# Kernel tuning notes

Hardware: AMD Instinct MI355X
Metric: run time of the kernel (lower is better)

The kernel has to match this reference:

```python
import jax, jax.numpy as jnp
import numpy as np

GRID_SIZE = 8
MARGIN = 1.0
NUM_NEG = 4
SOS_NEG = 8
LOSS_LAMBDA = 1.0
IMG_H, IMG_W = 960, 1280  # desc2 is the stride-GRID_SIZE feature map of this image
BIG = 5.0    # fill for radius-masked entries in FOS distance matrix (> max unit-desc dist 2)
HUGE = 1e6   # fill for invalid entries in SOS candidate scores


def _l2n(x, eps=1e-8):
    return x / (jnp.linalg.norm(x, axis=-1, keepdims=True) + eps)


def _pdist(a, b, eps=1e-12):
    # a: B x N x C, b: B x M x C -> B x N x M euclidean distances
    sq = (jnp.sum(a * a, -1)[..., :, None] + jnp.sum(b * b, -1)[..., None, :]
          - 2.0 * jnp.einsum('bnc,bmc->bnm', a, b))
    return jnp.sqrt(jnp.maximum(sq, eps))


def _bilinear(desc, pts):
    # desc: B x C x H x W, pts: B x N x 2 in (y, x) image-pixel coords -> B x N x C
    B, C, H, W = desc.shape
    g = pts / GRID_SIZE - 0.5  # image coords -> feature-grid coords
    gy = jnp.clip(g[..., 0], 0.0, H - 1.0)
    gx = jnp.clip(g[..., 1], 0.0, W - 1.0)
    y0 = jnp.clip(jnp.floor(gy).astype(jnp.int32), 0, H - 2)
    x0 = jnp.clip(jnp.floor(gx).astype(jnp.int32), 0, W - 2)
    wy = (gy - y0)[:, None, :]
    wx = (gx - x0)[:, None, :]
    flat = desc.reshape(B, C, H * W)
    gat = lambda yi, xi: jnp.take_along_axis(flat, (yi * W + xi)[:, None, :], axis=2)
    v00, v01 = gat(y0, x0), gat(y0, x0 + 1)
    v10, v11 = gat(y0 + 1, x0), gat(y0 + 1, x0 + 1)
    out = (v00 * (1 - wy) * (1 - wx) + v01 * (1 - wy) * wx
           + v10 * wy * (1 - wx) + v11 * wy * wx)
    return out.transpose(0, 2, 1)


def _forward(kp1, w_kp1, kp1_desc, desc2, homo12):
    r = 2.0 * GRID_SIZE  # spatial masking radius
    d1 = _l2n(kp1_desc)                       # B x N x C
    w_desc = _l2n(_bilinear(desc2, w_kp1))    # B x N x C interpolated warped descriptors

    # visibility of kp1 under homography homo12 (kp stored as (y, x))
    ones = jnp.ones_like(kp1[..., :1])
    p = jnp.concatenate([kp1[..., 1:2], kp1[..., 0:1], ones], -1)  # (x, y, 1)
    q = jnp.einsum('bij,bnj->bni', homo12, p)
    qx = q[..., 0] / (q[..., 2] + 1e-8)
    qy = q[..., 1] / (q[..., 2] + 1e-8)
    vis = ((qx >= 0) & (qx < IMG_W) & (qy >= 0) & (qy < IMG_H)).astype(d1.dtype)
    denom = jnp.sum(vis) + 1e-8

    # ---- FOS: hard quad triplet with radius masking ----
    pos = jnp.sqrt(jnp.sum((d1 - w_desc) ** 2, -1) + 1e-12)  # B x N
    D = _pdist(d1, w_desc)          # B x N x N cross descriptor distances
    s22 = _pdist(w_kp1, w_kp1)      # B x N x N warped-coordinate distances
    Dm = jnp.where(s22 <= r, BIG, D)  # mask spatial near-positives (incl. diagonal)
    neg1 = -jax.lax.top_k(-Dm, NUM_NEG)[0]                       # hardest negs per row anchor
    neg2 = -jax.lax.top_k(-Dm.transpose(0, 2, 1), NUM_NEG)[0]    # per column anchor
    t1 = jnp.mean(jax.nn.relu(MARGIN + pos[..., None] - neg1), -1)
    t2 = jnp.mean(jax.nn.relu(MARGIN + pos[..., None] - neg2), -1)
    fos = jnp.sum(vis * 0.5 * (t1 + t2)) / denom

    # ---- SOS: radius-masked second-order similarity regularizer ----
    s11 = _pdist(kp1, kp1)
    d11 = _pdist(d1, d1)
    d22 = _pdist(w_desc, w_desc)
    valid = (s11 > r) & (s22 > r)
    score = jnp.where(valid, d11, HUGE)
    nscore, idx = jax.lax.top_k(-score, SOS_NEG)  # sos_neg hardest valid neighbors
    sel_d11 = -nscore
    sel_d22 = jnp.take_along_axis(d22, idx, axis=2)
    diff2 = jnp.where(sel_d11 < HUGE * 0.1, (sel_d11 - sel_d22) ** 2, 0.0)
    sos_i = jnp.sqrt(jnp.sum(diff2, -1) + 1e-12)
    sos = jnp.sum(vis * sos_i) / denom

    return (fos + sos) * LOSS_LAMBDA


def setup_inputs() -> dict:
    key = jax.random.key(0)
    k1, k2, k3, k4, k5 = jax.random.split(key, 5)
    B, N, C, H, W = 2, 4096, 128, 120, 160
    scale = jnp.array([IMG_H - 1.0, IMG_W - 1.0], dtype=jnp.float32)
    kp1 = jax.random.uniform(k1, (B, N, 2), dtype=jnp.float32) * scale
    w_kp1 = jax.random.uniform(k2, (B, N, 2), dtype=jnp.float32) * scale
    kp1_desc = jax.random.normal(k3, (B, N, C), dtype=jnp.float32)
    desc2 = jax.random.normal(k4, (B, C, H, W), dtype=jnp.float32)
    homo12 = (jnp.tile(jnp.eye(3, dtype=jnp.float32), (B, 1, 1))
              + 0.001 * jax.random.normal(k5, (B, 3, 3), dtype=jnp.float32))
    return {'kp1': kp1, 'w_kp1': w_kp1, 'kp1_desc': kp1_desc,
            'desc2': desc2, 'homo12': homo12}


def reference(kp1, w_kp1, kp1_desc, desc2, homo12):
    return _forward(kp1, w_kp1, kp1_desc, desc2, homo12)
```

## Files before the change

### kernel.cpp

```cpp
#include <hip/hip_runtime.h>
#include <hip/hip_fp16.h>
#include <math.h>

#define NPTS 4096
#define CDIM 128
#define FH 120
#define FW 160
#define PIX (FH * FW)

typedef __attribute__((ext_vector_type(8))) short short8_t;
typedef __attribute__((ext_vector_type(4))) float float4_t;
typedef __attribute__((ext_vector_type(16))) float f32x16_t;
typedef __attribute__((ext_vector_type(2))) unsigned short ushort2_t;

#define OFF_FRAG  0
#define OFF_WDB   1048576
#define OFF_JA    1572864
#define OFF_JB    1605632
#define OFF_POS   1622016
#define OFF_VIS   1630208
#define OFF_ACC   1638400
#define OFF_D2T   2031632
#define OFF_PARTS 2031632
#define OFF_END   4489232

__device__ __forceinline__ unsigned short f2bf(float f) {
  unsigned int u = __float_as_uint(f);
  u = (u + 0x7fffu + ((u >> 16) & 1u)) >> 16;
  return (unsigned short)u;
}

__device__ __forceinline__ float wavesum(float v) {
#pragma unroll
  for (int off = 1; off < 64; off <<= 1) v += __shfl_xor(v, off, 64);
  return v;
}

typedef const __attribute__((address_space(1))) unsigned int gu32_t;
typedef __attribute__((address_space(3))) unsigned int lu32_t;
__device__ __forceinline__ void gl_lds16(const void* g, void* l) {
  __builtin_amdgcn_global_load_lds((gu32_t*)g, (lu32_t*)l, 16, 0, 0);
}

__global__ __launch_bounds__(256) void transpose_desc2(
    const float* __restrict__ d2, unsigned short* __restrict__ out) {
  __shared__ unsigned short tile[64][130];
  const int bp = blockIdx.x;
  const int b = bp / 300;
  const int p0 = (bp - b * 300) * 64;
  const int tid = threadIdx.x;
  const int grp = tid >> 6, lp = tid & 63;
#pragma unroll 4
  for (int r = 0; r < 32; ++r) {
    int c = (r << 2) | grp;
    float v = d2[((size_t)b * CDIM + c) * PIX + p0 + lp];
    tile[lp][c] = __half_as_ushort(__float2half(v));
  }
  __syncthreads();
  unsigned int* ob = (unsigned int*)(out + ((size_t)b * PIX + p0) * CDIM);
#pragma unroll
  for (int i = 0; i < 16; ++i) {
    int u = (i << 8) | tid;
    int p = u >> 6, cc = (u & 63) << 1;
    unsigned int lo = tile[p][cc], hi = tile[p][cc + 1];
    ob[u] = lo | (hi << 16);
  }
}

#define PREP_TAIL() do {                                                        \
  {                                                                             \
    const int pc = p & (NPTS - 1);                                              \
    const int Tc = pc >> 5, m = pc & 31;                                        \
    const int kq = lane >> 3, hi2 = (lane >> 2) & 1, j0 = (lane & 3) * 2;       \
    const size_t off = (size_t)kq * 512 + (m + 32 * hi2) * 8 + j0;              \
    const size_t cb = ((size_t)b * 128 + Tc) * 8192;                            \
    ushort2_t st; st.x = f2bf(d0); st.y = f2bf(d1v);                            \
    ushort2_t sw; sw.x = f2bf(e0); sw.y = f2bf(e1);                             \
    *(ushort2_t*)(frag + cb + off) = st;                                        \
    *(ushort2_t*)(frag + cb + 4096 + off) = sw;                                 \
    ushort2_t swr; swr.x = f2bf(e0); swr.y = f2bf(e1);                          \
    *(ushort2_t*)(wdb + (size_t)p * CDIM + c2) = swr;                           \
  }                                                                             \
  float dd0 = d0 - e0, dd1 = d1v - e1;                                          \
  float ssp = wavesum(dd0 * dd0 + dd1 * dd1);                                   \
  if (lane == 0) {                                                              \
    pos[p] = sqrtf(ssp + 1e-12f);                                               \
    float ky = kp1[p * 2 + 0], kx = kp1[p * 2 + 1];                             \
    jA[p] = make_float4(ky, kx, y, x);                                          \
    jb1[p] = -0.5f * n1;                                                        \
    jb2[p] = -0.5f * n2;                                                        \
    const float* h = homo + b * 9;                                              \
    float t0 = h[0] * kx + h[1] * ky + h[2];                                    \
    float t1 = h[3] * kx + h[4] * ky + h[5];                                    \
    float t2 = h[6] * kx + h[7] * ky + h[8];                                    \
    float qx = t0 / (t2 + 1e-8f), qy = t1 / (t2 + 1e-8f);                       \
    vis[p] = (qx >= 0.0f && qx < 1280.0f && qy >= 0.0f && qy < 960.0f)          \
                 ? 1.0f : 0.0f;                                                 \
  }                                                                             \
} while (0)

__global__ __launch_bounds__(256) void prep_t(
    const float* __restrict__ kp1, const float* __restrict__ wkp1,
    const float* __restrict__ desc, const unsigned short* __restrict__ d2t,
    const float* __restrict__ homo,
    unsigned short* __restrict__ frag, unsigned short* __restrict__ wdb,
    float4* __restrict__ jA, float* __restrict__ jb1, float* __restrict__ jb2,
    float* __restrict__ pos, float* __restrict__ vis, float* __restrict__ acc) {
  const int tid = threadIdx.x;
  if (blockIdx.x == 0 && tid < 4) acc[tid] = 0.0f;
  const int p = blockIdx.x * 4 + (tid >> 6);
  const int lane = tid & 63;
  const int b = p >> 12;
  const int c2 = lane * 2;

  float2 v = *(const float2*)(desc + (size_t)p * CDIM + c2);
  float ss = wavesum(v.x * v.x + v.y * v.y);
  float inv = 1.0f / (sqrtf(ss) + 1e-8f);
  float d0 = v.x * inv, d1v = v.y * inv;
  float n1 = ss * inv * inv;

  float y = wkp1[p * 2 + 0], x = wkp1[p * 2 + 1];
  float gy = fminf(fmaxf(y * 0.125f - 0.5f, 0.0f), (float)(FH - 1));
  float gx = fminf(fmaxf(x * 0.125f - 0.5f, 0.0f), (float)(FW - 1));
  int y0 = (int)floorf(gy); y0 = min(max(y0, 0), FH - 2);
  int x0 = (int)floorf(gx); x0 = min(max(x0, 0), FW - 2);
  float wy = gy - (float)y0, wx = gx - (float)x0;
  float w00 = (1 - wy) * (1 - wx), w01 = (1 - wy) * wx;
  float w10 = wy * (1 - wx), w11 = wy * wx;
  const unsigned int* t00 = (const unsigned int*)
      (d2t + ((size_t)b * PIX + y0 * FW + x0) * CDIM) + lane;
  unsigned int u00 = t00[0], u01 = t00[64];
  unsigned int u10 = t00[FW * 64], u11 = t00[FW * 64 + 64];
  float2 f00 = __half22float2(*(const __half2*)&u00);
  float2 f01 = __half22float2(*(const __half2*)&u01);
  float2 f10 = __half22float2(*(const __half2*)&u10);
  float2 f11 = __half22float2(*(const __half2*)&u11);
  float wv0 = f00.x * w00 + f01.x * w01 + f10.x * w10 + f11.x * w11;
  float wv1 = f00.y * w00 + f01.y * w01 + f10.y * w10 + f11.y * w11;
  float ss2 = wavesum(wv0 * wv0 + wv1 * wv1);
  float inv2 = 1.0f / (sqrtf(ss2) + 1e-8f);
  float e0 = wv0 * inv2, e1 = wv1 * inv2;
  float n2 = ss2 * inv2 * inv2;

  PREP_TAIL();
}

__global__ __launch_bounds__(256) void prep_g(
    const float* __restrict__ kp1, const float* __restrict__ wkp1,
    const float* __restrict__ desc, const float* __restrict__ desc2,
    const float* __restrict__ homo,
    unsigned short* __restrict__ frag, unsigned short* __restrict__ wdb,
    float4* __restrict__ jA, float* __restrict__ jb1, float* __restrict__ jb2,
    float* __restrict__ pos, float* __restrict__ vis, float* __restrict__ acc) {
  const int tid = threadIdx.x;
  if (blockIdx.x == 0 && tid < 4) acc[tid] = 0.0f;
  const int p = blockIdx.x * 4 + (tid >> 6);
  const int lane = tid & 63;
  const int b = p >> 12;
  const int c2 = lane * 2;

  float2 v = *(const float2*)(desc + (size_t)p * CDIM + c2);
  float ss = wavesum(v.x * v.x + v.y * v.y);
  float inv = 1.0f / (sqrtf(ss) + 1e-8f);
  float d0 = v.x * inv, d1v = v.y * inv;
  float n1 = ss * inv * inv;

  float y = wkp1[p * 2 + 0], x = wkp1[p * 2 + 1];
  float gy = fminf(fmaxf(y * 0.125f - 0.5f, 0.0f), (float)(FH - 1));
  float gx = fminf(fmaxf(x * 0.125f - 0.5f, 0.0f), (float)(FW - 1));
  int y0 = (int)floorf(gy); y0 = min(max(y0, 0), FH - 2);
  int x0 = (int)floorf(gx); x0 = min(max(x0, 0), FW - 2);
  float wy = gy - (float)y0, wx = gx - (float)x0;
  float w00 = (1 - wy) * (1 - wx), w01 = (1 - wy) * wx;
  float w10 = wy * (1 - wx), w11 = wy * wx;
  const float* q0 = desc2 + ((size_t)b * CDIM + c2) * PIX + y0 * FW + x0;
  const float* q1 = q0 + PIX;
  float wv0 = q0[0] * w00 + q0[1] * w01 + q0[FW] * w10 + q0[FW + 1] * w11;
  float wv1 = q1[0] * w00 + q1[1] * w01 + q1[FW] * w10 + q1[FW + 1] * w11;
  float ss2 = wavesum(wv0 * wv0 + wv1 * wv1);
  float inv2 = 1.0f / (sqrtf(ss2) + 1e-8f);
  float e0 = wv0 * inv2, e1 = wv1 * inv2;
  float n2 = ss2 * inv2 * inv2;

  PREP_TAIL();
}

__device__ __forceinline__ void ins6m(float v, float* L) {
  float p0 = L[0]; L[0] = fmaxf(L[0], v);
  float p1 = L[1]; L[1] = __builtin_amdgcn_fmed3f(p0, L[1], v);
  float p2 = L[2]; L[2] = __builtin_amdgcn_fmed3f(p1, L[2], v);
  float p3 = L[3]; L[3] = __builtin_amdgcn_fmed3f(p2, L[3], v);
  float p4 = L[4]; L[4] = __builtin_amdgcn_fmed3f(p3, L[4], v);
  L[5] = __builtin_amdgcn_fmed3f(p4, L[5], v);
}
__device__ __forceinline__ void ins8m(float v, float* L) {
  float p0 = L[0]; L[0] = fmaxf(L[0], v);
  float pk = p0;
#pragma unroll
  for (int k = 1; k < 7; ++k) {
    float cur = L[k];
    L[k] = __builtin_amdgcn_fmed3f(pk, cur, v);
    pk = cur;
  }
  L[7] = __builtin_amdgcn_fmed3f(pk, L[7], v);
}
__device__ __forceinline__ void ins12m(float v, float* L) {
  float p0 = L[0]; L[0] = fmaxf(L[0], v);
  float pk = p0;
#pragma unroll
  for (int k = 1; k < 11; ++k) {
    float cur = L[k];
    L[k] = __builtin_amdgcn_fmed3f(pk, cur, v);
    pk = cur;
  }
  L[11] = __builtin_amdgcn_fmed3f(pk, L[11], v);
}

__device__ __forceinline__ float packkey(float s, int j) {
  return __uint_as_float((__float_as_uint(s) & 0xFFFFF000u) | (unsigned)j);
}

#define CHUNK(T) do {                                                           \
  const unsigned short* bp = &buf[(T) & 3][0];                                  \
  float4 m1v[4], m2v[4];                                                        \
  _Pragma("unroll")                                                             \
  for (int q = 0; q < 4; ++q) {                                                 \
    m1v[q] = *(const float4*)&jbL[(T) * 32 + q * 8 + hi * 4];                   \
    m2v[q] = *(const float4*)&jbL[512 + (T) * 32 + q * 8 + hi * 4];             \
  }                                                                             \
  f32x16_t aD, aDt, a11;                                                        \
  _Pragma("unroll")                                                             \
  for (int q = 0; q < 4; ++q) {                                                 \
    _Pragma("unroll")                                                           \
    for (int i = 0; i < 4; ++i) {                                               \
      aD[q * 4 + i] = m2v[q][i];                                                \
      aDt[q * 4 + i] = m1v[q][i];                                               \
      a11[q * 4 + i] = m1v[q][i];                                               \
    }                                                                           \
  }                                                                             \
  __builtin_amdgcn_s_setprio(1);                                                \
  _Pragma("unroll")                                                             \
  for (int kq = 0; kq < 8; ++kq) {                                              \
    short8_t Ad = *(const short8_t*)(bp + kq * 512 + lane * 8);                 \
    short8_t Aw = *(const short8_t*)(bp + 4096 + kq * 512 + lane * 8);          \
    aD  = __builtin_amdgcn_mfma_f32_32x32x16_bf16(Aw, Bd[kq], aD,  0, 0, 0);    \
    aDt = __builtin_amdgcn_mfma_f32_32x32x16_bf16(Ad, Bw[kq], aDt, 0, 0, 0);    \
    a11 = __builtin_amdgcn_mfma_f32_32x32x16_bf16(Ad, Bd[kq], a11, 0, 0, 0);    \
  }                                                                             \
  __builtin_amdgcn_s_setprio(0);                                                \
  const int jjp = jbase + (T) * 32 + (hi << 2);                                 \
  _Pragma("unroll")                                                             \
  for (int reg = 0; reg < 16; ++reg) {                                          \
    const int jj = jjp | ((reg & 3) | ((reg >> 2) << 3));                       \
    ins6m(packkey(aD[reg], jj), fD);                                            \
    ins6m(packkey(aDt[reg], jj), fDt);                                          \
    ins8m(packkey(a11[reg], jj), fS);                                           \
  }                                                                             \
} while (0)

#define STAGE_C(BI, CT) do {                                                    \
  const unsigned short* gsrc =                                                  \
      fa + (size_t)(CT) * 8192 + wave * 512 + lane * 8;                         \
  _Pragma("unroll")                                                             \
  for (int i = 0; i < 4; ++i)                                                   \
    gl_lds16(gsrc + i * 2048, &buf[BI][i * 2048 + wave * 512]);                 \
} while (0)

__global__ __launch_bounds__(256, 2) void loss_main(
    const unsigned short* __restrict__ frag,
    const float* __restrict__ jb1g, const float* __restrict__ jb2g,
    float* __restrict__ parts) {
  __shared__ __align__(16) unsigned short buf[4][8192];
  __shared__ __align__(16) float jbL[1024];

  const int tid = threadIdx.x;
  const int bid = blockIdx.x;
  const int combo = ((bid & 7) << 1) | (bid >> 8);
  const int b   = combo >> 3;
  const int seg = combo & 7;
  const int g   = (bid >> 3) & 31;
  const int wave = tid >> 6, lane = tid & 63;
  const int hi = lane >> 5;
  const int base = b * NPTS;
  const int jbase = seg << 9;

  short8_t Bd[8], Bw[8];
  {
    const unsigned short* fb =
        frag + ((size_t)b * 128 + (g * 4 + wave)) * 8192 + (size_t)lane * 8;
#pragma unroll
    for (int kq = 0; kq < 8; ++kq) {
      Bd[kq] = *(const short8_t*)(fb + kq * 512);
      Bw[kq] = *(const short8_t*)(fb + 4096 + kq * 512);
    }
  }

  if (wave == 0) {
    gl_lds16(jb1g + base + jbase + lane * 4, &jbL[0]);
    gl_lds16(jb1g + base + jbase + 256 + lane * 4, &jbL[256]);
  } else if (wave == 1) {
    gl_lds16(jb2g + base + jbase + lane * 4, &jbL[512]);
    gl_lds16(jb2g + base + jbase + 256 + lane * 4, &jbL[768]);
  }

  float fD[6], fDt[6], fS[8];
#pragma unroll
  for (int k = 0; k < 6; ++k) { fD[k] = -1e30f; fDt[k] = -1e30f; }
#pragma unroll
  for (int k = 0; k < 8; ++k) fS[k] = -1e30f;

  const unsigned short* fa = frag + ((size_t)b * 128 + (jbase >> 5)) * 8192;

  STAGE_C(0, 0);
  STAGE_C(1, 1);
  STAGE_C(2, 2);
  asm volatile("s_waitcnt vmcnt(8)" ::: "memory");
  __builtin_amdgcn_s_barrier();
  asm volatile("" ::: "memory");

  for (int t = 0; t < 13; ++t) {
    STAGE_C((t + 3) & 3, t + 3);
    CHUNK(t);
    asm volatile("s_waitcnt vmcnt(8)" ::: "memory");
    __builtin_amdgcn_s_barrier();
    asm volatile("" ::: "memory");
  }
  CHUNK(13);
  asm volatile("s_waitcnt vmcnt(4)" ::: "memory");
  __builtin_amdgcn_s_barrier();
  asm volatile("" ::: "memory");
  CHUNK(14);
  asm volatile("s_waitcnt vmcnt(0)" ::: "memory");
  __builtin_amdgcn_s_barrier();
  asm volatile("" ::: "memory");
  CHUNK(15);

  float eD[8], eDt[8], eS[12];
#pragma unroll
  for (int k = 0; k < 6; ++k) { eD[k] = fD[k]; eDt[k] = fDt[k]; }
  eD[6] = eD[7] = eDt[6] = eDt[7] = -1e30f;
#pragma unroll
  for (int k = 0; k < 8; ++k) eS[k] = fS[k];
  eS[8] = eS[9] = eS[10] = eS[11] = -1e30f;
#pragma unroll
  for (int k = 0; k < 6; ++k) ins8m(__shfl_xor(fD[k], 32, 64), eD);
#pragma unroll
  for (int k = 0; k < 6; ++k) ins8m(__shfl_xor(fDt[k], 32, 64), eDt);
#pragma unroll
  for (int k = 0; k < 8; ++k) ins12m(__shfl_xor(fS[k], 32, 64), eS);

  if (lane < 32) {
    float* P = parts + (size_t)(seg * 28) * 8192 +
               (base + g * 128 + wave * 32 + lane);
#pragma unroll
    for (int k = 0; k < 8; ++k) {
      P[(size_t)k * 8192] = eD[k];
      P[(size_t)(8 + k) * 8192] = eDt[k];
    }
#pragma unroll
    for (int k = 0; k < 12; ++k) P[(size_t)(16 + k) * 8192] = eS[k];
  }
}

__device__ __forceinline__ float bflo(unsigned int u) { return __uint_as_float(u << 16); }
__device__ __forceinline__ float bfhi(unsigned int u) { return __uint_as_float(u & 0xFFFF0000u); }

__global__ __launch_bounds__(256) void merge_filter(
    const float* __restrict__ parts, const float4* __restrict__ jAg,
    const float* __restrict__ jb1g, const float* __restrict__ jb2g,
    const float* __restrict__ posg,
    const float* __restrict__ visg, const unsigned short* __restrict__ wdb,
    float* __restrict__ accum, float* __restrict__ out) {
  __shared__ int sJ[256];
  __shared__ float sD11[256], sD22[256], sT[64], sVis[32], sN2[32];
  const int tid = threadIdx.x;
  const int a0 = blockIdx.x * 32;

  if (tid < 64) {
    const int al = tid & 31;
    const int type = tid >> 5;
    const int a = a0 + al;
    const int base = a & ~(NPTS - 1);
    float L[8];
#pragma unroll
    for (int k = 0; k < 8; ++k) L[k] = -1e30f;
    const float* P = parts + (size_t)(type * 8) * 8192 + a;
#pragma unroll
    for (int s = 0; s < 8; ++s) {
#pragma unroll
      for (int k = 0; k < 8; ++k) ins8m(P[(size_t)(s * 28 + k) * 8192], L);
    }
    const float4 own = jAg[a];
    const float pv = posg[a];
    const float nsel = -2.0f * (type ? jb2g[a] : jb1g[a]);
    float ts = 0.0f;
    int got = 0;
#pragma unroll
    for (int k = 0; k < 8; ++k) {
      int j = (int)(__float_as_uint(L[k]) & 0xFFFu);
      float4 jc = jAg[base + j];
      float dz = own.z - jc.z, dw = own.w - jc.w;
      if (got < 4 && dz * dz + dw * dw > 256.0f) {
        float d2 = fmaf(-2.0f, L[k], nsel);
        ts += fmaxf(1.0f + pv - sqrtf(fmaxf(d2, 1e-12f)), 0.0f);
        got++;
      }
    }
    sT[tid] = ts;
  } else if (tid < 96) {
    const int al = tid - 64;
    const int a = a0 + al;
    const int base = a & ~(NPTS - 1);
    float S[12];
#pragma unroll
    for (int k = 0; k < 12; ++k) S[k] = -1e30f;
    const float* P = parts + a;
#pragma unroll
    for (int s = 0; s < 8; ++s) {
#pragma unroll
      for (int k = 0; k < 12; ++k) ins12m(P[(size_t)(s * 28 + 16 + k) * 8192], S);
    }
    const float4 own = jAg[a];
    const float n1i = -2.0f * jb1g[a];
    int m = 0;
#pragma unroll
    for (int k = 0; k < 12; ++k) {
      int j = (int)(__float_as_uint(S[k]) & 0xFFFu);
      float4 jc = jAg[base + j];
      float ay = own.x - jc.x, ax = own.y - jc.y;
      float wz = own.z - jc.z, ww = own.w - jc.w;
      if (m < 8 && ay * ay + ax * ax > 256.0f && wz * wz + ww * ww > 256.0f) {
        sJ[al * 8 + m] = base + j;
        sD11[al * 8 + m] = sqrtf(fmaxf(fmaf(-2.0f, S[k], n1i), 1e-12f));
        m++;
      }
    }
    for (int k = m; k < 8; ++k) sJ[al * 8 + k] = -1;
    sVis[al] = visg[a];
    sN2[al] = -2.0f * jb2g[a];
  }
  __syncthreads();

  {
    const int slot = tid;
    const int al = slot >> 3;
    const int j = sJ[slot];
    float d22 = 0.0f;
    if (j >= 0) {
      const uint4* pi = (const uint4*)(wdb + (size_t)(a0 + al) * CDIM);
      const uint4* pj = (const uint4*)(wdb + (size_t)j * CDIM);
      float dot = 0.0f;
#pragma unroll
      for (int qq = 0; qq < 16; ++qq) {
        uint4 ui = pi[qq], uj = pj[qq];
        dot = fmaf(bflo(ui.x), bflo(uj.x), dot); dot = fmaf(bfhi(ui.x), bfhi(uj.x), dot);
        dot = fmaf(bflo(ui.y), bflo(uj.y), dot); dot = fmaf(bfhi(ui.y), bfhi(uj.y), dot);
        dot = fmaf(bflo(ui.z), bflo(uj.z), dot); dot = fmaf(bfhi(ui.z), bfhi(uj.z), dot);
        dot = fmaf(bflo(ui.w), bflo(uj.w), dot); dot = fmaf(bfhi(ui.w), bfhi(uj.w), dot);
      }
      d22 = sqrtf(fmaxf(fmaf(-2.0f, jb2g[j] + dot, sN2[al]), 1e-12f));
    }
    sD22[slot] = d22;
  }
  __syncthreads();

  float contrib = 0.0f, vsum = 0.0f;
  if (tid < 32) {
    float s = 0.0f;
#pragma unroll
    for (int k = 0; k < 8; ++k) {
      if (sJ[tid * 8 + k] >= 0) {
        float d = sD11[tid * 8 + k] - sD22[tid * 8 + k];
        s = fmaf(d, d, s);
      }
    }
    contrib = sVis[tid] * (0.125f * (sT[tid] + sT[32 + tid]) + sqrtf(s + 1e-12f));
    vsum = sVis[tid];
  }
  if (tid < 64) {
#pragma unroll
    for (int off = 32; off >= 1; off >>= 1) {
      contrib += __shfl_down(contrib, off, 64);
      vsum += __shfl_down(vsum, off, 64);
    }
    if (tid == 0) {
      atomicAdd(&accum[0], contrib);
      atomicAdd(&accum[1], vsum);
      __threadfence();
      float old = atomicAdd(&accum[2], 1.0f);
      if (old == 255.0f) {
        float t = atomicAdd(&accum[0], 0.0f);
        float v = atomicAdd(&accum[1], 0.0f);
        out[0] = t / (v + 1e-8f);
      }
    }
  }
}

extern "C" void kernel_launch(void* const* d_in, const int* in_sizes, int n_in,
                              void* d_out, int out_size, void* d_ws, size_t ws_size,
                              hipStream_t stream) {
  (void)in_sizes; (void)n_in; (void)out_size;
  const float* kp1   = (const float*)d_in[0];
  const float* wkp1  = (const float*)d_in[1];
  const float* desc  = (const float*)d_in[2];
  const float* desc2 = (const float*)d_in[3];
  const float* homo  = (const float*)d_in[4];
  float* ws = (float*)d_ws;
  unsigned short* frag = (unsigned short*)(ws + OFF_FRAG);
  unsigned short* wdb  = (unsigned short*)(ws + OFF_WDB);
  float4* jA = (float4*)(ws + OFF_JA);
  float* jb1 = ws + OFF_JB;
  float* jb2 = ws + OFF_JB + 8192;
  float* pos = ws + OFF_POS;
  float* vis = ws + OFF_VIS;
  float* acc = ws + OFF_ACC;
  float* parts = ws + OFF_PARTS;
  unsigned short* d2t = (unsigned short*)(ws + OFF_D2T);

  if (ws_size >= (size_t)OFF_END * 4) {
    transpose_desc2<<<600, 256, 0, stream>>>(desc2, d2t);
    prep_t<<<2048, 256, 0, stream>>>(kp1, wkp1, desc, d2t, homo,
                                     frag, wdb, jA, jb1, jb2, pos, vis, acc);
  } else {
    prep_g<<<2048, 256, 0, stream>>>(kp1, wkp1, desc, desc2, homo,
                                     frag, wdb, jA, jb1, jb2, pos, vis, acc);
  }
  loss_main<<<512, 256, 0, stream>>>(frag, jb1, jb2, parts);
  merge_filter<<<256, 256, 0, stream>>>(parts, jA, jb1, jb2, pos, vis, wdb, acc,
                                        (float*)d_out);
}
```

Measured before the change: 152.0 us.

## Split loss_main column sweep across two wave halves with LDS top-k merge

Doubles the block to 512 threads so two groups of four waves each process half of the 16 column chunks for the same row tile, then merges their partial top-k lists through shared memory before writing. The staging changes from a 4-deep single-stream ring to double buffering per half, with full block barriers. This is meant to add wave-level parallelism and latency hiding per CU, at the cost of extra register-resident B fragments per wave, a shared-memory merge step, and more register pressure under the launch bound of 512 threads and 4 blocks.

```diff
diff --git a/kernel.cpp b/kernel.cpp
--- a/kernel.cpp
+++ b/kernel.cpp
@@ -220,8 +220,8 @@
   return __uint_as_float((__float_as_uint(s) & 0xFFFFF000u) | (unsigned)j);
 }
 
-#define CHUNK(T) do {                                                           \
-  const unsigned short* bp = &buf[(T) & 3][0];                                  \
+#define CHUNK(T, BP) do {                                                       \
+  const unsigned short* bp = (BP);                                              \
   float4 m1v[4], m2v[4];                                                        \
   _Pragma("unroll")                                                             \
   for (int q = 0; q < 4; ++q) {                                                 \
@@ -258,15 +258,17 @@
   }                                                                             \
 } while (0)
 
-#define STAGE_C(BI, CT) do {                                                    \
-  const unsigned short* gsrc =                                                  \
-      fa + (size_t)(CT) * 8192 + wave * 512 + lane * 8;                         \
-  _Pragma("unroll")                                                             \
-  for (int i = 0; i < 4; ++i)                                                   \
-    gl_lds16(gsrc + i * 2048, &buf[BI][i * 2048 + wave * 512]);                 \
+#define STAGE_S(S) do {                                                         \
+  const int sl = (S) & 1;                                                       \
+  const unsigned short* g0 = fa + (size_t)(S) * 8192 + wave * 1024 + lane * 8;  \
+  const unsigned short* g1 = g0 + 8 * 8192;                                     \
+  gl_lds16(g0, &buf[sl][wave * 1024]);                                          \
+  gl_lds16(g0 + 512, &buf[sl][wave * 1024 + 512]);                              \
+  gl_lds16(g1, &buf[2 + sl][wave * 1024]);                                      \
+  gl_lds16(g1 + 512, &buf[2 + sl][wave * 1024 + 512]);                          \
 } while (0)
 
-__global__ __launch_bounds__(256, 2) void loss_main(
+__global__ __launch_bounds__(512, 4) void loss_main(
     const unsigned short* __restrict__ frag,
     const float* __restrict__ jb1g, const float* __restrict__ jb2g,
     float* __restrict__ parts) {
@@ -280,6 +282,8 @@
   const int seg = combo & 7;
   const int g   = (bid >> 3) & 31;
   const int wave = tid >> 6, lane = tid & 63;
+  const int half = wave >> 2;
+  const int aw   = wave & 3;
   const int hi = lane >> 5;
   const int base = b * NPTS;
   const int jbase = seg << 9;
@@ -287,7 +291,7 @@
   short8_t Bd[8], Bw[8];
   {
     const unsigned short* fb =
-        frag + ((size_t)b * 128 + (g * 4 + wave)) * 8192 + (size_t)lane * 8;
+        frag + ((size_t)b * 128 + (g * 4 + aw)) * 8192 + (size_t)lane * 8;
 #pragma unroll
     for (int kq = 0; kq < 8; ++kq) {
       Bd[kq] = *(const short8_t*)(fb + kq * 512);
@@ -311,29 +315,15 @@
 
   const unsigned short* fa = frag + ((size_t)b * 128 + (jbase >> 5)) * 8192;
 
-  STAGE_C(0, 0);
-  STAGE_C(1, 1);
-  STAGE_C(2, 2);
-  asm volatile("s_waitcnt vmcnt(8)" ::: "memory");
-  __builtin_amdgcn_s_barrier();
-  asm volatile("" ::: "memory");
-
-  for (int t = 0; t < 13; ++t) {
-    STAGE_C((t + 3) & 3, t + 3);
-    CHUNK(t);
-    asm volatile("s_waitcnt vmcnt(8)" ::: "memory");
-    __builtin_amdgcn_s_barrier();
-    asm volatile("" ::: "memory");
-  }
-  CHUNK(13);
-  asm volatile("s_waitcnt vmcnt(4)" ::: "memory");
-  __builtin_amdgcn_s_barrier();
-  asm volatile("" ::: "memory");
-  CHUNK(14);
-  asm volatile("s_waitcnt vmcnt(0)" ::: "memory");
-  __builtin_amdgcn_s_barrier();
-  asm volatile("" ::: "memory");
-  CHUNK(15);
+  STAGE_S(0);
+  __syncthreads();
+
+  for (int s = 0; s < 7; ++s) {
+    STAGE_S(s + 1);
+    CHUNK(half * 8 + s, &buf[half * 2 + (s & 1)][0]);
+    __syncthreads();
+  }
+  CHUNK(half * 8 + 7, &buf[half * 2 + 1][0]);
 
   float eD[8], eDt[8], eS[12];
 #pragma unroll
@@ -349,9 +339,27 @@
 #pragma unroll
   for (int k = 0; k < 8; ++k) ins12m(__shfl_xor(fS[k], 32, 64), eS);
 
-  if (lane < 32) {
+  __syncthreads();
+  float* mb = (float*)&buf[0][0];
+  if (half == 1 && lane < 32) {
+    float* m = mb + (aw * 32 + lane) * 29;
+#pragma unroll
+    for (int k = 0; k < 8; ++k) { m[k] = eD[k]; m[8 + k] = eDt[k]; }
+#pragma unroll
+    for (int k = 0; k < 12; ++k) m[16 + k] = eS[k];
+  }
+  __syncthreads();
+  if (half == 0 && lane < 32) {
+    const float* m = mb + (aw * 32 + lane) * 29;
+#pragma unroll
+    for (int k = 0; k < 8; ++k) ins8m(m[k], eD);
+#pragma unroll
+    for (int k = 0; k < 8; ++k) ins8m(m[8 + k], eDt);
+#pragma unroll
+    for (int k = 0; k < 12; ++k) ins12m(m[16 + k], eS);
+
     float* P = parts + (size_t)(seg * 28) * 8192 +
-               (base + g * 128 + wave * 32 + lane);
+               (base + g * 128 + aw * 32 + lane);
 #pragma unroll
     for (int k = 0; k < 8; ++k) {
       P[(size_t)k * 8192] = eD[k];
@@ -526,7 +534,7 @@
     prep_g<<<2048, 256, 0, stream>>>(kp1, wkp1, desc, desc2, homo,
                                      frag, wdb, jA, jb1, jb2, pos, vis, acc);
   }
-  loss_main<<<512, 256, 0, stream>>>(frag, jb1, jb2, parts);
+  loss_main<<<512, 512, 0, stream>>>(frag, jb1, jb2, parts);
   merge_filter<<<256, 256, 0, stream>>>(parts, jA, jb1, jb2, pos, vis, wdb, acc,
                                         (float*)d_out);
 }
```

Result: slower. 164.7 us (+8.3%).

## Fuse merge/filter stage into loss kernel via last-block-per-group counters

Applied to the files above, without the earlier changes.

The separate merge_filter launch is removed. In loss_main, the last of the 8 blocks finishing each row group, detected with an atomic counter, now performs the top-k merge, SOS filtering and the final reduction for its 128 anchors, reusing LDS. This saves one kernel launch and lets the merge work overlap with the tail of the main stage. In exchange, the merge work is concentrated in 64 blocks (128 anchors each) rather than spread over 256 blocks, which may lengthen the tail.

```diff
diff --git a/kernel.cpp b/kernel.cpp
--- a/kernel.cpp
+++ b/kernel.cpp
@@ -107,7 +107,7 @@
     float4* __restrict__ jA, float* __restrict__ jb1, float* __restrict__ jb2,
     float* __restrict__ pos, float* __restrict__ vis, float* __restrict__ acc) {
   const int tid = threadIdx.x;
-  if (blockIdx.x == 0 && tid < 4) acc[tid] = 0.0f;
+  if (blockIdx.x == 0 && tid < 96) acc[tid] = 0.0f;
   const int p = blockIdx.x * 4 + (tid >> 6);
   const int lane = tid & 63;
   const int b = p >> 12;
@@ -153,7 +153,7 @@
     float4* __restrict__ jA, float* __restrict__ jb1, float* __restrict__ jb2,
     float* __restrict__ pos, float* __restrict__ vis, float* __restrict__ acc) {
   const int tid = threadIdx.x;
-  if (blockIdx.x == 0 && tid < 4) acc[tid] = 0.0f;
+  if (blockIdx.x == 0 && tid < 96) acc[tid] = 0.0f;
   const int p = blockIdx.x * 4 + (tid >> 6);
   const int lane = tid & 63;
   const int b = p >> 12;
@@ -219,6 +219,9 @@
 __device__ __forceinline__ float packkey(float s, int j) {
   return __uint_as_float((__float_as_uint(s) & 0xFFFFF000u) | (unsigned)j);
 }
+
+__device__ __forceinline__ float bflo(unsigned int u) { return __uint_as_float(u << 16); }
+__device__ __forceinline__ float bfhi(unsigned int u) { return __uint_as_float(u & 0xFFFF0000u); }
 
 #define CHUNK(T) do {                                                           \
   const unsigned short* bp = &buf[(T) & 3][0];                                  \
@@ -266,12 +269,16 @@
     gl_lds16(gsrc + i * 2048, &buf[BI][i * 2048 + wave * 512]);                 \
 } while (0)
 
-__global__ __launch_bounds__(256, 2) void loss_main(
+__global__ __launch_bounds__(256, 2) void loss_fused(
     const unsigned short* __restrict__ frag,
     const float* __restrict__ jb1g, const float* __restrict__ jb2g,
-    float* __restrict__ parts) {
+    const float4* __restrict__ jAg, const float* __restrict__ posg,
+    const float* __restrict__ visg, const unsigned short* __restrict__ wdb,
+    float* __restrict__ parts, float* __restrict__ accw,
+    float* __restrict__ out) {
   __shared__ __align__(16) unsigned short buf[4][8192];
   __shared__ __align__(16) float jbL[1024];
+  __shared__ int lastBlk;
 
   const int tid = threadIdx.x;
   const int bid = blockIdx.x;
@@ -360,27 +367,30 @@
 #pragma unroll
     for (int k = 0; k < 12; ++k) P[(size_t)(16 + k) * 8192] = eS[k];
   }
-}
-
-__device__ __forceinline__ float bflo(unsigned int u) { return __uint_as_float(u << 16); }
-__device__ __forceinline__ float bfhi(unsigned int u) { return __uint_as_float(u & 0xFFFF0000u); }
-
-__global__ __launch_bounds__(256) void merge_filter(
-    const float* __restrict__ parts, const float4* __restrict__ jAg,
-    const float* __restrict__ jb1g, const float* __restrict__ jb2g,
-    const float* __restrict__ posg,
-    const float* __restrict__ visg, const unsigned short* __restrict__ wdb,
-    float* __restrict__ accum, float* __restrict__ out) {
-  __shared__ int sJ[256];
-  __shared__ float sD11[256], sD22[256], sT[64], sVis[32], sN2[32];
-  const int tid = threadIdx.x;
-  const int a0 = blockIdx.x * 32;
-
-  if (tid < 64) {
-    const int al = tid & 31;
-    const int type = tid >> 5;
-    const int a = a0 + al;
-    const int base = a & ~(NPTS - 1);
+
+  __threadfence();
+  __syncthreads();
+  if (tid == 0) {
+    float old = atomicAdd(&accw[16 + ((b << 5) | g)], 1.0f);
+    lastBlk = (old == 7.0f) ? 1 : 0;
+  }
+  __syncthreads();
+  if (!lastBlk) return;
+  __threadfence();
+
+  const int a0g = base + g * 128;
+  float* shf  = (float*)&buf[0][0];
+  int*   sJ   = (int*)shf;
+  float* sD11 = shf + 1024;
+  float* sD22 = shf + 2048;
+  float* sT   = shf + 3072;
+  float* sVis = shf + 3328;
+  float* sN2  = shf + 3456;
+  float* sRed = shf + 3584;
+
+  {
+    const int type = tid >> 7, al = tid & 127;
+    const int a = a0g + al;
     float L[8];
 #pragma unroll
     for (int k = 0; k < 8; ++k) L[k] = -1e30f;
@@ -406,11 +416,11 @@
         got++;
       }
     }
-    sT[tid] = ts;
-  } else if (tid < 96) {
-    const int al = tid - 64;
-    const int a = a0 + al;
-    const int base = a & ~(NPTS - 1);
+    sT[type * 128 + al] = ts;
+  }
+  if (tid < 128) {
+    const int al = tid;
+    const int a = a0g + al;
     float S[12];
 #pragma unroll
     for (int k = 0; k < 12; ++k) S[k] = -1e30f;
@@ -418,7 +428,8 @@
 #pragma unroll
     for (int s = 0; s < 8; ++s) {
 #pragma unroll
-      for (int k = 0; k < 12; ++k) ins12m(P[(size_t)(s * 28 + 16 + k) * 8192], S);
+      for (int k = 0; k < 12; ++k)
+        ins12m(P[(size_t)(s * 28 + 16 + k) * 8192], S);
     }
     const float4 own = jAg[a];
     const float n1i = -2.0f * jb1g[a];
@@ -441,13 +452,12 @@
   }
   __syncthreads();
 
-  {
-    const int slot = tid;
-    const int al = slot >> 3;
-    const int j = sJ[slot];
+  for (int sl = tid; sl < 1024; sl += 256) {
+    const int al = sl >> 3;
+    const int j = sJ[sl];
     float d22 = 0.0f;
     if (j >= 0) {
-      const uint4* pi = (const uint4*)(wdb + (size_t)(a0 + al) * CDIM);
+      const uint4* pi = (const uint4*)(wdb + (size_t)(a0g + al) * CDIM);
       const uint4* pj = (const uint4*)(wdb + (size_t)j * CDIM);
       float dot = 0.0f;
 #pragma unroll
@@ -460,12 +470,12 @@
       }
       d22 = sqrtf(fmaxf(fmaf(-2.0f, jb2g[j] + dot, sN2[al]), 1e-12f));
     }
-    sD22[slot] = d22;
+    sD22[sl] = d22;
   }
   __syncthreads();
 
   float contrib = 0.0f, vsum = 0.0f;
-  if (tid < 32) {
+  if (tid < 128) {
     float s = 0.0f;
 #pragma unroll
     for (int k = 0; k < 8; ++k) {
@@ -474,25 +484,27 @@
         s = fmaf(d, d, s);
       }
     }
-    contrib = sVis[tid] * (0.125f * (sT[tid] + sT[32 + tid]) + sqrtf(s + 1e-12f));
+    contrib = sVis[tid] * (0.125f * (sT[tid] + sT[128 + tid]) + sqrtf(s + 1e-12f));
     vsum = sVis[tid];
   }
-  if (tid < 64) {
-#pragma unroll
-    for (int off = 32; off >= 1; off >>= 1) {
-      contrib += __shfl_down(contrib, off, 64);
-      vsum += __shfl_down(vsum, off, 64);
-    }
-    if (tid == 0) {
-      atomicAdd(&accum[0], contrib);
-      atomicAdd(&accum[1], vsum);
-      __threadfence();
-      float old = atomicAdd(&accum[2], 1.0f);
-      if (old == 255.0f) {
-        float t = atomicAdd(&accum[0], 0.0f);
-        float v = atomicAdd(&accum[1], 0.0f);
-        out[0] = t / (v + 1e-8f);
-      }
+#pragma unroll
+  for (int off = 32; off >= 1; off >>= 1) {
+    contrib += __shfl_down(contrib, off, 64);
+    vsum += __shfl_down(vsum, off, 64);
+  }
+  __syncthreads();
+  if (tid == 64) { sRed[0] = contrib; sRed[1] = vsum; }
+  __syncthreads();
+  if (tid == 0) {
+    contrib += sRed[0]; vsum += sRed[1];
+    atomicAdd(&accw[0], contrib);
+    atomicAdd(&accw[1], vsum);
+    __threadfence();
+    float old = atomicAdd(&accw[2], 1.0f);
+    if (old == 63.0f) {
+      float t = atomicAdd(&accw[0], 0.0f);
+      float v = atomicAdd(&accw[1], 0.0f);
+      out[0] = t / (v + 1e-8f);
     }
   }
 }
@@ -526,7 +538,6 @@
     prep_g<<<2048, 256, 0, stream>>>(kp1, wkp1, desc, desc2, homo,
                                      frag, wdb, jA, jb1, jb2, pos, vis, acc);
   }
-  loss_main<<<512, 256, 0, stream>>>(frag, jb1, jb2, parts);
-  merge_filter<<<256, 256, 0, stream>>>(parts, jA, jb1, jb2, pos, vis, wdb, acc,
-                                        (float*)d_out);
-}
+  loss_fused<<<512, 256, 0, stream>>>(frag, jb1, jb2, jA, pos, vis, wdb,
+                                      parts, acc, (float*)d_out);
+}
```

Result: slower. 222.7 us (+46.5%).
